# Kernel tuning notes

Hardware: AMD Instinct MI355X
Metric: run time of the kernel (lower is better)

Reference implementation:

```python
import jax, jax.numpy as jnp
import numpy as np

B, N, M = 2, 4096, 4096
QUERY_DIM = 1024
CONTEXT_DIM = 1024
HEADS = 16
DIM_HEAD = 64
INNER = HEADS * DIM_HEAD


def setup_inputs() -> dict:
    key = jax.random.key(0)
    ks = jax.random.split(key, 7)
    s = 0.02
    return {
        "x": jax.random.normal(ks[0], (B, N, QUERY_DIM), dtype=jnp.float32),
        "context": jax.random.normal(ks[1], (B, M, CONTEXT_DIM), dtype=jnp.float32),
        "Wq": jax.random.normal(ks[2], (QUERY_DIM, INNER), dtype=jnp.float32) * s,
        "Wk": jax.random.normal(ks[3], (CONTEXT_DIM, INNER), dtype=jnp.float32) * s,
        "Wv": jax.random.normal(ks[4], (CONTEXT_DIM, INNER), dtype=jnp.float32) * s,
        "Wo": jax.random.normal(ks[5], (INNER, QUERY_DIM), dtype=jnp.float32) * s,
        "bo": jnp.zeros((QUERY_DIM,), dtype=jnp.float32),
    }


def reference(x, context, Wq, Wk, Wv, Wo, bo):
    scale = DIM_HEAD ** -0.5
    # projections, then split heads: b n (h d) -> b h n d
    q = (x @ Wq).reshape(B, N, HEADS, DIM_HEAD).transpose(0, 2, 1, 3)
    k = (context @ Wk).reshape(B, M, HEADS, DIM_HEAD).transpose(0, 2, 1, 3)
    v = (context @ Wv).reshape(B, M, HEADS, DIM_HEAD).transpose(0, 2, 1, 3)
    attn = jnp.einsum('bhnd,bhmd->bhnm', q, k) * scale  # [B,H,N,M]
    attn = jax.nn.softmax(attn, axis=-1)
    out = jnp.einsum('bhnm,bhmd->bhnd', attn, v)
    out = out.transpose(0, 2, 1, 3).reshape(B, N, INNER)  # b h n d -> b n (h d)
    return out @ Wo + bo  # dropout(p=0) is identity
```

## Files before the change

### kernel.cpp

```cpp
#include <hip/hip_runtime.h>

using f16    = _Float16;
using f16x2  = __attribute__((ext_vector_type(2))) _Float16;
using f16x4  = __attribute__((ext_vector_type(4))) _Float16;
using f16x8  = __attribute__((ext_vector_type(8))) _Float16;
using h16x2  = __attribute__((ext_vector_type(2))) __fp16;
using f32x4  = __attribute__((ext_vector_type(4))) float;
using f32x16 = __attribute__((ext_vector_type(16))) float;
using u32    = unsigned int;
using u32x4  = __attribute__((ext_vector_type(4))) u32;

#define DI __device__ __forceinline__

DI f16x4 pack4(float a, float b, float c, float d) {
  f16x2 lo = __builtin_bit_cast(f16x2, __builtin_amdgcn_cvt_pkrtz(a, b));
  f16x2 hi = __builtin_bit_cast(f16x2, __builtin_amdgcn_cvt_pkrtz(c, d));
  f16x4 r; r[0] = lo[0]; r[1] = lo[1]; r[2] = hi[0]; r[3] = hi[1];
  return r;
}

DI u32 pk32(float a, float b) {
  return __builtin_bit_cast(u32, __builtin_amdgcn_cvt_pkrtz(a, b));
}

DI float dot1(u32 wrd, float acc) {
#if __has_builtin(__builtin_amdgcn_fdot2)
  h16x2 one; one[0] = (__fp16)1.f; one[1] = (__fp16)1.f;
  return __builtin_amdgcn_fdot2(__builtin_bit_cast(h16x2, wrd), one, acc, false);
#else
  f16x2 p = __builtin_bit_cast(f16x2, wrd);
  return acc + (float)p[0] + (float)p[1];
#endif
}

DI void gll16(const void* g, void* l) {
  __builtin_amdgcn_global_load_lds((const __attribute__((address_space(1))) u32*)g,
                                   (__attribute__((address_space(3))) u32*)l, 16, 0, 0);
}

DI f16x8 ldfrag(const void* base, int row, int u4) {
  int phys = u4 ^ (row & 7);
  return *(const f16x8*)((const char*)base + row * 128 + phys * 16);
}

DI f16x8 ldsc(const void* base, int row, int slot) {
  return *(const f16x8*)((const char*)base + slot * 1024 + row * 16);
}

DI f32x4 mfma16(f16x8 a, f16x8 b, f32x4 c) {
  return __builtin_amdgcn_mfma_f32_16x16x32_f16(a, b, c, 0, 0, 0);
}
DI f32x16 mfma32(f16x8 a, f16x8 b, f32x16 c) {
  return __builtin_amdgcn_mfma_f32_32x32x16_f16(a, b, c, 0, 0, 0);
}

DI void softhalf(const f32x16& s, f16x8* bp2, float& lr) {
  f32x16 e;
#pragma unroll
  for (int i = 0; i < 16; ++i) e[i] = __builtin_amdgcn_exp2f(s[i]);
  u32 a[8];
#pragma unroll
  for (int i = 0; i < 8; ++i) a[i] = pk32(e[2 * i], e[2 * i + 1]);
  float s0 = lr;
#pragma unroll
  for (int i = 0; i < 8; ++i) s0 = dot1(a[i], s0);
  lr = s0;
  auto s02 = __builtin_amdgcn_permlane32_swap(a[0], a[2], false, false);
  auto s13 = __builtin_amdgcn_permlane32_swap(a[1], a[3], false, false);
  auto s46 = __builtin_amdgcn_permlane32_swap(a[4], a[6], false, false);
  auto s57 = __builtin_amdgcn_permlane32_swap(a[5], a[7], false, false);
  u32x4 w0 = {s02[0], s13[0], s02[1], s13[1]};
  u32x4 w1 = {s46[0], s57[0], s46[1], s57[1]};
  bp2[0] = __builtin_bit_cast(f16x8, w0);
  bp2[1] = __builtin_bit_cast(f16x8, w1);
}

__global__ void k_cvt2(const float* __restrict__ x, const float* __restrict__ ctx,
                       f16* __restrict__ dst, int n4) {
  int z = blockIdx.y;
  const float* s = z ? ctx : x;
  f16* d = dst + (size_t)z * 8192 * 1024;
  int i = blockIdx.x * blockDim.x + threadIdx.x;
  if (i < n4) {
    float4 v = ((const float4*)s)[i];
    ((f16x4*)d)[i] = pack4(v.x, v.y, v.z, v.w);
  }
}

__global__ void k_wt4(const float* __restrict__ Wq, const float* __restrict__ Wk,
                      const float* __restrict__ Wv, const float* __restrict__ Wo,
                      f16* __restrict__ WTb) {
  int z = blockIdx.z;
  const float* W = z == 0 ? Wq : z == 1 ? Wk : z == 2 ? Wv : Wo;
  f16* WT = WTb + (size_t)z * 1024 * 1024;
  __shared__ float tile[64][65];
  int k0 = blockIdx.y * 64, n0 = blockIdx.x * 64;
  int t = threadIdx.x;
#pragma unroll
  for (int p = 0; p < 4; ++p) {
    int r = p * 16 + (t >> 4);
    int c = (t & 15) * 4;
    float4 v = *(const float4*)&W[(size_t)(k0 + r) * 1024 + n0 + c];
    tile[r][c] = v.x; tile[r][c + 1] = v.y; tile[r][c + 2] = v.z; tile[r][c + 3] = v.w;
  }
  __syncthreads();
#pragma unroll
  for (int p = 0; p < 4; ++p) {
    int n = p * 16 + (t >> 4);
    int k = (t & 15) * 4;
    *(f16x4*)&WT[(size_t)(n0 + n) * 1024 + k0 + k] =
        pack4(tile[k][n], tile[k + 1][n], tile[k + 2][n], tile[k + 3][n]);
  }
}

template <int EPI>
__global__ __launch_bounds__(256) void k_gemm(const f16* __restrict__ A, const f16* __restrict__ Bt,
                                              void* __restrict__ Cp, const float* __restrict__ bias) {
  __shared__ __align__(16) char smem[65536];
  f16* sA = (f16*)smem;
  f16* sB = (f16*)(smem + 32768);
  const int tid = threadIdx.x, w = tid >> 6, lane = tid & 63;
  const int g = lane >> 4, l15 = lane & 15, l7 = lane & 7, l8 = lane >> 3;
  const int m0 = blockIdx.x * 128, n0 = blockIdx.y * 128;
  const int wm = w >> 1, wn = w & 1;
  const int uswz = l7 ^ l8;

  auto stage = [&](int kt, int bufi) {
    int kb = kt * 128;
#pragma unroll
    for (int q = 0; q < 4; ++q) {
      int row = w * 32 + q * 8 + l8;
      gll16((const char*)A + (size_t)(m0 + row) * 2048 + kb + uswz * 16,
            (char*)sA + bufi * 16384 + (w * 32 + q * 8) * 128);
      gll16((const char*)Bt + (size_t)(n0 + row) * 2048 + kb + uswz * 16,
            (char*)sB + bufi * 16384 + (w * 32 + q * 8) * 128);
    }
  };

  f32x4 acc[4][4] = {};
  stage(0, 0);
  for (int kt = 0; kt < 16; ++kt) {
    asm volatile("s_waitcnt vmcnt(0)" ::: "memory");
    __syncthreads();
    if (kt + 1 < 16) stage(kt + 1, (kt + 1) & 1);
    const f16* aL = (const f16*)((const char*)sA + (kt & 1) * 16384);
    const f16* bL = (const f16*)((const char*)sB + (kt & 1) * 16384);
#pragma unroll
    for (int kc = 0; kc < 2; ++kc) {
      f16x8 af[4], bf[4];
#pragma unroll
      for (int mi = 0; mi < 4; ++mi) af[mi] = ldfrag(aL, wm * 64 + mi * 16 + l15, kc * 4 + g);
#pragma unroll
      for (int ni = 0; ni < 4; ++ni) bf[ni] = ldfrag(bL, wn * 64 + ni * 16 + l15, kc * 4 + g);
#pragma unroll
      for (int mi = 0; mi < 4; ++mi)
#pragma unroll
        for (int ni = 0; ni < 4; ++ni) acc[mi][ni] = mfma16(af[mi], bf[ni], acc[mi][ni]);
    }
  }

  if (EPI == 2) {
    float* C = (float*)Cp;
    float bv[4];
#pragma unroll
    for (int ni = 0; ni < 4; ++ni) bv[ni] = bias[n0 + wn * 64 + ni * 16 + l15];
#pragma unroll
    for (int mi = 0; mi < 4; ++mi)
#pragma unroll
      for (int ni = 0; ni < 4; ++ni) {
        int col = n0 + wn * 64 + ni * 16 + l15;
#pragma unroll
        for (int i = 0; i < 4; ++i) {
          int row = m0 + wm * 64 + mi * 16 + g * 4 + i;
          C[(size_t)row * 1024 + col] = acc[mi][ni][i] + bv[ni];
        }
      }
    return;
  }

  __syncthreads();
  f16* Ct = (f16*)smem;
  if (EPI == 0 || EPI == 3) {
#pragma unroll
    for (int mi = 0; mi < 4; ++mi)
#pragma unroll
      for (int ni = 0; ni < 4; ++ni) {
        int col = wn * 64 + ni * 16 + l15;
#pragma unroll
        for (int i = 0; i < 4; ++i) Ct[(wm * 64 + mi * 16 + g * 4 + i) * 136 + col] = (f16)acc[mi][ni][i];
      }
    __syncthreads();
    if (EPI == 0) {
      f16* C = (f16*)Cp;
#pragma unroll
      for (int p = 0; p < 8; ++p) {
        int r = p * 16 + (tid >> 4), cu = tid & 15;
        f16x8 v = *(const f16x8*)((const char*)Ct + r * 272 + cu * 16);
        *(f16x8*)((char*)C + (size_t)(m0 + r) * 2048 + n0 * 2 + cu * 16) = v;
      }
    } else {
      int b = m0 >> 12, mmr = m0 & 4095;
#pragma unroll
      for (int p = 0; p < 8; ++p) {
        int r = p * 16 + (tid >> 4), cu = tid & 15;
        f16x8 v = *(const f16x8*)((const char*)Ct + r * 272 + cu * 16);
        int kvr = mmr + r;
        int h = (n0 >> 6) + (cu >> 3);
        size_t off = ((size_t)((b * 16 + h) * 64 + (kvr >> 6))) * 8192 + (cu & 7) * 1024 + (kvr & 63) * 16;
        *(f16x8*)((char*)Cp + off) = v;
      }
    }
  } else {
#pragma unroll
    for (int mi = 0; mi < 4; ++mi)
#pragma unroll
      for (int ni = 0; ni < 4; ++ni) {
        int n = wn * 64 + ni * 16 + l15;
        int mcol = wm * 64 + mi * 16 + g * 4;
        *(f16x4*)&Ct[n * 136 + mcol] =
            pack4(acc[mi][ni][0], acc[mi][ni][1], acc[mi][ni][2], acc[mi][ni][3]);
      }
    __syncthreads();
    int b = m0 >> 12, mm = m0 & 4095;
#pragma unroll
    for (int p = 0; p < 8; ++p) {
      int r = p * 16 + (tid >> 4), cu = tid & 15;
      f16x8 v = *(const f16x8*)((const char*)Ct + r * 272 + cu * 16);
      int h = (n0 + r) >> 6, d = (n0 + r) & 63;
      size_t off = ((size_t)((b * 16 + h) * 64 + (mm >> 6) + (cu >> 3))) * 8192 + (cu & 7) * 1024 + d * 16;
      *(f16x8*)((char*)Cp + off) = v;
    }
  }
}

__global__ __launch_bounds__(512, 4) void k_attn(const f16* __restrict__ Qh, const f16* __restrict__ Ks,
                                                 const f16* __restrict__ Vs, f16* __restrict__ Oh) {
  __shared__ __align__(16) char smem[32768];
  const int tid = threadIdx.x, w = tid >> 6, lane = tid & 63;
  const int hi = lane >> 5, c = lane & 31, l7 = lane & 7, l8 = lane >> 3;
  const int bid = blockIdx.x;
  const int bh = (bid & 7) * 4 + (bid >> 7);
  const int qc = (bid >> 3) & 15;
  const int b = bh >> 4, h = bh & 15;
  const int rowB = b * 4096;
  const int qrow0 = rowB + qc * 256 + w * 32;
  const size_t tb = (size_t)bh * 64 * 8192;

  const f16 ce = (f16)0.18033688f;
  f16x8 bQ[4];
#pragma unroll
  for (int ks = 0; ks < 4; ++ks) {
    f16x8 r0 = *(const f16x8*)(Qh + (size_t)(qrow0 + c) * 1024 + h * 64 + ks * 16 + hi * 8);
#pragma unroll
    for (int e = 0; e < 8; ++e) r0[e] *= ce;
    bQ[ks] = r0;
  }

  const f32x16 Z = {};
  f32x16 acc0 = {}, acc1 = {};
  float lrow = 0.f;

  auto stage = [&](int t, int bufi) {
    const char* gK = (const char*)Ks + tb + (size_t)t * 8192 + w * 1024 + lane * 16;
    const char* gV = (const char*)Vs + tb + (size_t)t * 8192 + w * 1024 + lane * 16;
    gll16(gK, (char*)smem + bufi * 8192 + w * 1024);
    gll16(gV, (char*)smem + 16384 + bufi * 8192 + w * 1024);
  };

  stage(0, 0);
#pragma unroll 1
  for (int t = 0; t < 64; ++t) {
    asm volatile("s_waitcnt vmcnt(0)" ::: "memory");
    __syncthreads();
    if (t + 1 < 64) stage(t + 1, (t + 1) & 1);
    const char* Kl = (const char*)smem + (t & 1) * 8192;
    const char* Vl = (const char*)smem + 16384 + (t & 1) * 8192;

    f16x8 kf[8];
#pragma unroll
    for (int ks = 0; ks < 4; ++ks) {
      kf[ks * 2]     = ldsc(Kl, c, ks * 2 + hi);
      kf[ks * 2 + 1] = ldsc(Kl, 32 + c, ks * 2 + hi);
    }

    __builtin_amdgcn_s_setprio(1);
    f32x16 st0 = mfma32(kf[0], bQ[0], Z);
    f32x16 st1 = mfma32(kf[1], bQ[0], Z);
#pragma unroll
    for (int ks = 1; ks < 4; ++ks) {
      st0 = mfma32(kf[ks * 2], bQ[ks], st0);
      st1 = mfma32(kf[ks * 2 + 1], bQ[ks], st1);
    }
    __builtin_amdgcn_s_setprio(0);
    __builtin_amdgcn_sched_barrier(0);

    f16x8 vf[8];
#pragma unroll
    for (int ks = 0; ks < 4; ++ks) {
      vf[ks * 2]     = ldsc(Vl, c, ks * 2 + hi);
      vf[ks * 2 + 1] = ldsc(Vl, 32 + c, ks * 2 + hi);
    }

    f16x8 bp[4];
    softhalf(st0, &bp[0], lrow);
    softhalf(st1, &bp[2], lrow);

    __builtin_amdgcn_s_setprio(1);
#pragma unroll
    for (int ks = 0; ks < 4; ++ks) {
      acc0 = mfma32(vf[ks * 2], bp[ks], acc0);
      acc1 = mfma32(vf[ks * 2 + 1], bp[ks], acc1);
    }
    __builtin_amdgcn_s_setprio(0);
  }

  float inv;
  {
    auto r2 = __builtin_amdgcn_permlane32_swap(__builtin_bit_cast(u32, lrow),
                                               __builtin_bit_cast(u32, lrow), false, false);
    inv = 1.0f / (__builtin_bit_cast(float, r2[0]) + __builtin_bit_cast(float, r2[1]));
  }

  __syncthreads();
  char* myO = (char*)smem + w * 4096;
  int r = c;
#pragma unroll
  for (int dt = 0; dt < 2; ++dt) {
    const f32x16& A = dt ? acc1 : acc0;
#pragma unroll
    for (int q8 = 0; q8 < 4; ++q8) {
      f16x4 hv = pack4(A[q8 * 4] * inv, A[q8 * 4 + 1] * inv, A[q8 * 4 + 2] * inv, A[q8 * 4 + 3] * inv);
      int slot = dt * 4 + q8;
      *(f16x4*)(myO + r * 128 + ((slot ^ (r & 7)) * 16) + hi * 8) = hv;
    }
  }
#pragma unroll
  for (int p = 0; p < 4; ++p) {
    int rr = p * 8 + l8;
    f16x8 v = *(const f16x8*)(myO + rr * 128 + ((l7 ^ (rr & 7)) * 16));
    *(f16x8*)((char*)Oh + ((size_t)(qrow0 + rr) * 1024 + h * 64) * 2 + l7 * 16) = v;
  }
}

extern "C" void kernel_launch(void* const* d_in, const int* in_sizes, int n_in,
                              void* d_out, int out_size, void* d_ws, size_t ws_size,
                              hipStream_t stream) {
  const float* x   = (const float*)d_in[0];
  const float* ctx = (const float*)d_in[1];
  const float* Wq  = (const float*)d_in[2];
  const float* Wk  = (const float*)d_in[3];
  const float* Wv  = (const float*)d_in[4];
  const float* Wo  = (const float*)d_in[5];
  const float* bo  = (const float*)d_in[6];
  float* out = (float*)d_out;

  const size_t NR = 8192, KD = 1024;
  if (ws_size < (size_t)(5 * NR * KD * 2 + 4 * KD * KD * 2)) return;

  char* ws = (char*)d_ws;
  f16* xh  = (f16*)ws;
  f16* ch  = xh + NR * KD;
  f16* WqT = ch + NR * KD;
  f16* WkT = WqT + KD * KD;
  f16* WvT = WkT + KD * KD;
  f16* WoT = WvT + KD * KD;
  f16* Qh  = WoT + KD * KD;
  f16* Ks  = Qh + NR * KD;
  f16* Vs  = Ks + NR * KD;
  f16* Oh  = xh;

  int n4 = (int)(NR * KD / 4);
  k_cvt2<<<dim3((n4 + 255) / 256, 2), dim3(256), 0, stream>>>(x, ctx, xh, n4);
  k_wt4<<<dim3(16, 16, 4), dim3(256), 0, stream>>>(Wq, Wk, Wv, Wo, WqT);

  dim3 gg(64, 8), gb(256);
  k_gemm<0><<<gg, gb, 0, stream>>>(xh, WqT, (void*)Qh, nullptr);
  k_gemm<3><<<gg, gb, 0, stream>>>(ch, WkT, (void*)Ks, nullptr);
  k_gemm<1><<<gg, gb, 0, stream>>>(ch, WvT, (void*)Vs, nullptr);

  k_attn<<<dim3(512), dim3(512), 0, stream>>>(Qh, Ks, Vs, Oh);

  k_gemm<2><<<gg, gb, 0, stream>>>(Oh, WoT, (void*)out, bo);
}
```

Measured before the change: 290.4 us.

## Halve attention block size to 4 waves and split PV into two softmax halves

The attention kernel now runs 1024 blocks of 256 threads (4 waves, 128 query rows each) instead of 512 blocks of 512 threads. Each wave stages two 1 KB chunks of K and V per tile to keep the same 8 KB tile per block. The PV loop is split into two halves, each loading only the V fragments it needs right after its softmax half, which lowers register pressure and interleaves the exp work with the MFMAs. The trade-off is that each K/V tile is read from global memory by twice as many blocks, doubling K/V traffic, in exchange for more blocks per CU and better load balance.

```diff
diff --git a/kernel.cpp b/kernel.cpp
--- a/kernel.cpp
+++ b/kernel.cpp
@@ -233,17 +233,17 @@
   }
 }
 
-__global__ __launch_bounds__(512, 4) void k_attn(const f16* __restrict__ Qh, const f16* __restrict__ Ks,
+__global__ __launch_bounds__(256, 4) void k_attn(const f16* __restrict__ Qh, const f16* __restrict__ Ks,
                                                  const f16* __restrict__ Vs, f16* __restrict__ Oh) {
   __shared__ __align__(16) char smem[32768];
   const int tid = threadIdx.x, w = tid >> 6, lane = tid & 63;
   const int hi = lane >> 5, c = lane & 31, l7 = lane & 7, l8 = lane >> 3;
   const int bid = blockIdx.x;
-  const int bh = (bid & 7) * 4 + (bid >> 7);
-  const int qc = (bid >> 3) & 15;
+  const int bh = (bid & 7) * 4 + (bid >> 8);
+  const int qc = (bid >> 3) & 31;
   const int b = bh >> 4, h = bh & 15;
   const int rowB = b * 4096;
-  const int qrow0 = rowB + qc * 256 + w * 32;
+  const int qrow0 = rowB + qc * 128 + w * 32;
   const size_t tb = (size_t)bh * 64 * 8192;
 
   const f16 ce = (f16)0.18033688f;
@@ -261,10 +261,14 @@
   float lrow = 0.f;
 
   auto stage = [&](int t, int bufi) {
-    const char* gK = (const char*)Ks + tb + (size_t)t * 8192 + w * 1024 + lane * 16;
-    const char* gV = (const char*)Vs + tb + (size_t)t * 8192 + w * 1024 + lane * 16;
-    gll16(gK, (char*)smem + bufi * 8192 + w * 1024);
-    gll16(gV, (char*)smem + 16384 + bufi * 8192 + w * 1024);
+    const char* gK = (const char*)Ks + tb + (size_t)t * 8192 + w * 2048 + lane * 16;
+    const char* gV = (const char*)Vs + tb + (size_t)t * 8192 + w * 2048 + lane * 16;
+    char* dK = (char*)smem + bufi * 8192 + w * 2048;
+    char* dV = (char*)smem + 16384 + bufi * 8192 + w * 2048;
+    gll16(gK, dK);
+    gll16(gK + 1024, dK + 1024);
+    gll16(gV, dV);
+    gll16(gV + 1024, dV + 1024);
   };
 
   stage(0, 0);
@@ -294,24 +298,34 @@
     __builtin_amdgcn_s_setprio(0);
     __builtin_amdgcn_sched_barrier(0);
 
-    f16x8 vf[8];
-#pragma unroll
-    for (int ks = 0; ks < 4; ++ks) {
-      vf[ks * 2]     = ldsc(Vl, c, ks * 2 + hi);
-      vf[ks * 2 + 1] = ldsc(Vl, 32 + c, ks * 2 + hi);
-    }
-
-    f16x8 bp[4];
-    softhalf(st0, &bp[0], lrow);
-    softhalf(st1, &bp[2], lrow);
-
-    __builtin_amdgcn_s_setprio(1);
-#pragma unroll
-    for (int ks = 0; ks < 4; ++ks) {
-      acc0 = mfma32(vf[ks * 2], bp[ks], acc0);
-      acc1 = mfma32(vf[ks * 2 + 1], bp[ks], acc1);
-    }
-    __builtin_amdgcn_s_setprio(0);
+    {
+      f16x8 v0 = ldsc(Vl, c, hi);
+      f16x8 v1 = ldsc(Vl, 32 + c, hi);
+      f16x8 v2 = ldsc(Vl, c, 2 + hi);
+      f16x8 v3 = ldsc(Vl, 32 + c, 2 + hi);
+      f16x8 bp[2];
+      softhalf(st0, bp, lrow);
+      __builtin_amdgcn_s_setprio(1);
+      acc0 = mfma32(v0, bp[0], acc0);
+      acc1 = mfma32(v1, bp[0], acc1);
+      acc0 = mfma32(v2, bp[1], acc0);
+      acc1 = mfma32(v3, bp[1], acc1);
+      __builtin_amdgcn_s_setprio(0);
+    }
+    {
+      f16x8 v0 = ldsc(Vl, c, 4 + hi);
+      f16x8 v1 = ldsc(Vl, 32 + c, 4 + hi);
+      f16x8 v2 = ldsc(Vl, c, 6 + hi);
+      f16x8 v3 = ldsc(Vl, 32 + c, 6 + hi);
+      f16x8 bp[2];
+      softhalf(st1, bp, lrow);
+      __builtin_amdgcn_s_setprio(1);
+      acc0 = mfma32(v0, bp[0], acc0);
+      acc1 = mfma32(v1, bp[0], acc1);
+      acc0 = mfma32(v2, bp[1], acc0);
+      acc1 = mfma32(v3, bp[1], acc1);
+      __builtin_amdgcn_s_setprio(0);
+    }
   }
 
   float inv;
@@ -378,7 +392,7 @@
   k_gemm<3><<<gg, gb, 0, stream>>>(ch, WkT, (void*)Ks, nullptr);
   k_gemm<1><<<gg, gb, 0, stream>>>(ch, WvT, (void*)Vs, nullptr);
 
-  k_attn<<<dim3(512), dim3(512), 0, stream>>>(Qh, Ks, Vs, Oh);
+  k_attn<<<dim3(1024), dim3(256), 0, stream>>>(Qh, Ks, Vs, Oh);
 
   k_gemm<2><<<gg, gb, 0, stream>>>(Oh, WoT, (void*)out, bo);
 }
```

Result: faster. 277.6 us (-4.4%).
